# Performance work log

Measured on AMD Instinct MI355X. Metric: run time of the kernel, lower is better.

The kernel has to match this reference:

```python
import jax, jax.numpy as jnp
import numpy as np

B, N, CIN, H, UNITS = 8, 2048, 256, 256, 256


def setup_inputs() -> dict:
    key = jax.random.key(0)
    ks = jax.random.split(key, 7)
    s = 1.0 / np.sqrt(CIN)
    return {
        "x": jax.random.normal(ks[0], (B, N, CIN), dtype=jnp.float32),
        "Wq": jax.random.normal(ks[1], (CIN, H), dtype=jnp.float32) * s,
        "bq": jax.random.normal(ks[2], (H,), dtype=jnp.float32) * 0.01,
        "Wk": jax.random.normal(ks[3], (CIN, H), dtype=jnp.float32) * s,
        "bk": jax.random.normal(ks[4], (H,), dtype=jnp.float32) * 0.01,
        "Wm": jax.random.normal(ks[5], (H, UNITS), dtype=jnp.float32) * (1.0 / np.sqrt(H)),
        "bm": jax.random.normal(ks[6], (UNITS,), dtype=jnp.float32) * 0.01,
    }


def reference(x, Wq, bq, Wk, bk, Wm, bm):
    # Dense projections with fused relu (as in the Keras module)
    q = jax.nn.relu(x @ Wq + bq)          # (B,N,H)
    k = jax.nn.relu(x @ Wk + bk)          # (B,N,H)
    v = q                                 # NOTE: source uses fc_query for value (fc_value unused)
    # Unscaled key @ query^T, softmax over last axis
    kq = jax.nn.softmax(jnp.einsum('bnh,bmh->bnm', k, q), axis=-1)  # (B,N,N)
    # value^T @ kq, then Permute((2,1)): att[b,m,h] = sum_n v[b,n,h] * kq[b,n,m]
    att = jnp.einsum('bnh,bnm->bmh', v, kq)                          # (B,N,H)
    return jax.nn.relu(att @ Wm + bm)                                # (B,N,UNITS)
```

## Files before the change

kernel.cpp:

```cpp
#include <hip/hip_runtime.h>
#include <hip/hip_bf16.h>
#include <math.h>

#define BB   8
#define NN   2048
#define CC   256
#define MTOT (BB * NN)

typedef __bf16 bf16_t;
typedef bf16_t    bf16x8 __attribute__((ext_vector_type(8)));
typedef _Float16  halfx8 __attribute__((ext_vector_type(8)));
typedef float     floatx4 __attribute__((ext_vector_type(4)));

#define LOG2E 1.44269504088896f

__device__ __forceinline__ void gl_lds16(const bf16_t* g, bf16_t* l) {
    __builtin_amdgcn_global_load_lds(
        (const __attribute__((address_space(1))) unsigned int*)g,
        (__attribute__((address_space(3))) unsigned int*)l, 16, 0, 0);
}

template<int OMODE, bool BIASRELU, bool DO_STATS>
__global__ __launch_bounds__(256, 3)
void gemm_nt(const bf16_t* __restrict__ A, const bf16_t* __restrict__ B,
             void* __restrict__ C, const float* __restrict__ bias,
             int lda, int ldb, int ldc,
             long strideA, long strideB, long strideC,
             float* __restrict__ pm, float* __restrict__ pl)
{
    const int b = blockIdx.z;
    A += (long)b * strideA;
    B += (long)b * strideB;
    const int m0 = blockIdx.y * 128;
    const int n0 = blockIdx.x * 128;

    __shared__ bf16_t As[128 * 32];
    __shared__ bf16_t Bs[128 * 32];
    __shared__ float  smx[4][4][16];
    __shared__ float  ssm[4][4][16];

    const int tid  = threadIdx.x;
    const int wid  = tid >> 6, lane = tid & 63;
    const int wm   = (wid >> 1) * 64, wn = (wid & 1) * 64;
    const int fr   = lane & 15;
    const int kb   = (lane >> 4) * 8;

    floatx4 acc[4][4] = {};

    for (int k0 = 0; k0 < 256; k0 += 32) {
#pragma unroll
        for (int r = 0; r < 2; ++r) {
            const int lin = tid + r * 256;
            const int rw  = lin >> 2, kc = lin & 3;
            gl_lds16(A + (long)(m0 + rw) * lda + k0 + kc * 8, As + lin * 8);
            gl_lds16(B + (long)(n0 + rw) * ldb + k0 + kc * 8, Bs + lin * 8);
        }
        __syncthreads();
        bf16x8 af[4], bf[4];
#pragma unroll
        for (int f = 0; f < 4; ++f) {
            af[f] = *(const bf16x8*)(As + (wm + f * 16 + fr) * 32 + kb);
            bf[f] = *(const bf16x8*)(Bs + (wn + f * 16 + fr) * 32 + kb);
        }
#pragma unroll
        for (int f = 0; f < 4; ++f)
#pragma unroll
            for (int g = 0; g < 4; ++g)
                acc[f][g] = __builtin_amdgcn_mfma_f32_16x16x32_bf16(af[f], bf[g], acc[f][g], 0, 0, 0);
        __syncthreads();
    }

    const int rbase = (lane >> 4) * 4;
#pragma unroll
    for (int g = 0; g < 4; ++g) {
        const int n = n0 + wn + g * 16 + fr;
        const float bv = BIASRELU ? bias[n] : 0.0f;
#pragma unroll
        for (int f = 0; f < 4; ++f) {
#pragma unroll
            for (int r = 0; r < 4; ++r) {
                const int m = m0 + wm + f * 16 + rbase + r;
                float v = acc[f][g][r] + bv;
                if (BIASRELU) v = v > 0.0f ? v : 0.0f;
                if (OMODE == 0)
                    ((float*)C)[(long)b * strideC + (long)m * ldc + n] = v;
                else if (OMODE == 1)
                    ((bf16_t*)C)[(long)b * strideC + (long)m * ldc + n] = (bf16_t)v;
                else
                    ((_Float16*)C)[(long)b * strideC + (long)m * ldc + n] = (_Float16)v;
            }
        }
    }

    if (DO_STATS) {
        float lmax[4], lsum[4];
#pragma unroll
        for (int g = 0; g < 4; ++g) {
            float m = -1e30f;
#pragma unroll
            for (int f = 0; f < 4; ++f)
#pragma unroll
                for (int r = 0; r < 4; ++r) m = fmaxf(m, acc[f][g][r]);
            m = fmaxf(m, __shfl_xor(m, 16));
            m = fmaxf(m, __shfl_xor(m, 32));
            float s = 0.0f;
#pragma unroll
            for (int f = 0; f < 4; ++f)
#pragma unroll
                for (int r = 0; r < 4; ++r) s += __expf(acc[f][g][r] - m);
            s += __shfl_xor(s, 16);
            s += __shfl_xor(s, 32);
            lmax[g] = m; lsum[g] = s;
        }
        if (lane < 16) {
#pragma unroll
            for (int g = 0; g < 4; ++g) {
                smx[wid][g][lane] = lmax[g];
                ssm[wid][g][lane] = lsum[g];
            }
        }
        __syncthreads();
        if (tid < 128) {
            const int pair = tid >> 6;
            const int idx  = tid & 63;
            const int g = idx >> 4, f2 = idx & 15;
            const float m0v = smx[pair][g][f2], m1v = smx[pair + 2][g][f2];
            const float M = fmaxf(m0v, m1v);
            const float L = ssm[pair][g][f2] * __expf(m0v - M) +
                            ssm[pair + 2][g][f2] * __expf(m1v - M);
            const int n = n0 + pair * 64 + g * 16 + f2;
            const long o = ((long)b * 16 + blockIdx.y) * NN + n;
            pm[o] = M;
            pl[o] = L;
        }
    }
}

__global__ __launch_bounds__(256)
void stats_combine(const float* __restrict__ pm, const float* __restrict__ pl,
                   float* __restrict__ c2)
{
    const int i = blockIdx.x * 256 + threadIdx.x;
    const int b = i >> 11, n = i & 2047;
    float M = -1e30f, L = 0.0f;
#pragma unroll
    for (int t = 0; t < 16; ++t) {
        const long o = ((long)b * 16 + t) * NN + n;
        const float m = pm[o], l = pl[o];
        const float nm = fmaxf(M, m);
        L = L * __expf(M - nm) + l * __expf(m - nm);
        M = nm;
    }
    c2[i] = (M + logf(L)) * LOG2E;
}

#define APAD 68
__global__ __launch_bounds__(256, 4)
void att_out(const _Float16* __restrict__ St, const bf16_t* __restrict__ qmT,
             const float* __restrict__ c2, const float* __restrict__ bm,
             float* __restrict__ out)
{
    const int b  = blockIdx.z;
    const int m0 = blockIdx.x * 32;
    const int u0 = blockIdx.y * 128;
    const _Float16* S  = St  + (long)b * NN * NN;
    const bf16_t*   Q  = qmT + (long)b * 256 * NN;
    const float*    C2 = c2  + b * NN;
    float*          O  = out + (long)b * NN * 256;

    __shared__ bf16_t As[32 * APAD];
    __shared__ bf16_t Bs[128 * 64];

    const int tid  = threadIdx.x;
    const int wid  = tid >> 6, lane = tid & 63;
    const int wm2  = (wid >> 1) * 16;
    const int wu   = (wid & 1) * 64;
    const int fr   = lane & 15;
    const int u16  = lane >> 4;
    const int kb   = u16 * 8;
    const int fsw  = fr & 7;
    const int arow = tid >> 3;
    const int aseg = tid & 7;

    const _Float16* Srow = S + (long)(m0 + arow) * NN + aseg * 8;

    floatx4 acc[4] = {};

    for (int n0 = 0; n0 < NN; n0 += 64) {
#pragma unroll
        for (int r = 0; r < 4; ++r) {
            const int lin = tid + r * 256;
            const int rw  = lin >> 3, kc = lin & 7;
            const int kcs = kc ^ (rw & 7);
            gl_lds16(Q + (long)(u0 + rw) * NN + n0 + kcs * 8, Bs + lin * 8);
        }
        const halfx8 hv = *(const halfx8*)(Srow + n0);
        const float4 ca = *(const float4*)(C2 + n0 + aseg * 8);
        const float4 cb = *(const float4*)(C2 + n0 + aseg * 8 + 4);
        bf16x8 p;
        p[0] = (bf16_t)exp2f(fmaf((float)hv[0], LOG2E, -ca.x));
        p[1] = (bf16_t)exp2f(fmaf((float)hv[1], LOG2E, -ca.y));
        p[2] = (bf16_t)exp2f(fmaf((float)hv[2], LOG2E, -ca.z));
        p[3] = (bf16_t)exp2f(fmaf((float)hv[3], LOG2E, -ca.w));
        p[4] = (bf16_t)exp2f(fmaf((float)hv[4], LOG2E, -cb.x));
        p[5] = (bf16_t)exp2f(fmaf((float)hv[5], LOG2E, -cb.y));
        p[6] = (bf16_t)exp2f(fmaf((float)hv[6], LOG2E, -cb.z));
        p[7] = (bf16_t)exp2f(fmaf((float)hv[7], LOG2E, -cb.w));
        *(bf16x8*)(As + arow * APAD + aseg * 8) = p;
        __syncthreads();

        bf16x8 af[2], bg[4][2];
#pragma unroll
        for (int j = 0; j < 2; ++j)
            af[j] = *(const bf16x8*)(As + (wm2 + fr) * APAD + j * 32 + kb);
#pragma unroll
        for (int g = 0; g < 4; ++g)
#pragma unroll
            for (int j = 0; j < 2; ++j) {
                const int chunk = (j * 4 + u16) ^ fsw;
                bg[g][j] = *(const bf16x8*)(Bs + (wu + g * 16 + fr) * 64 + chunk * 8);
            }
#pragma unroll
        for (int j = 0; j < 2; ++j)
#pragma unroll
            for (int g = 0; g < 4; ++g)
                acc[g] = __builtin_amdgcn_mfma_f32_16x16x32_bf16(af[j], bg[g][j], acc[g], 0, 0, 0);
        __syncthreads();
    }

    const int rbase = u16 * 4;
#pragma unroll
    for (int g = 0; g < 4; ++g) {
        const int u = u0 + wu + g * 16 + fr;
        const float bvv = bm[u];
#pragma unroll
        for (int r = 0; r < 4; ++r) {
            const int m = m0 + wm2 + rbase + r;
            const float v = acc[g][r] + bvv;
            O[(long)m * 256 + u] = v > 0.0f ? v : 0.0f;
        }
    }
}

__global__ __launch_bounds__(256)
void cvt_bf16(const float* __restrict__ x, bf16_t* __restrict__ y)
{
    const long i = ((long)blockIdx.x * 256 + threadIdx.x) * 8;
    const float4 a = *(const float4*)(x + i);
    const float4 b = *(const float4*)(x + i + 4);
    bf16x8 o;
    o[0] = (bf16_t)a.x; o[1] = (bf16_t)a.y; o[2] = (bf16_t)a.z; o[3] = (bf16_t)a.w;
    o[4] = (bf16_t)b.x; o[5] = (bf16_t)b.y; o[6] = (bf16_t)b.z; o[7] = (bf16_t)b.w;
    *(bf16x8*)(y + i) = o;
}

__global__ __launch_bounds__(256)
void prep_w(const float* __restrict__ Wq, const float* __restrict__ Wk,
            const float* __restrict__ Wm, const float* __restrict__ bq,
            const float* __restrict__ bk, bf16_t* __restrict__ WqkT,
            bf16_t* __restrict__ WmT, float* __restrict__ bqk)
{
    const int z = blockIdx.z;
    const float* W = (z == 0) ? Wq : (z == 1) ? Wk : Wm;
    bf16_t* Wt = (z == 0) ? WqkT : (z == 1) ? (WqkT + 256 * 256) : WmT;
    __shared__ float t[32][33];
    const int n0 = blockIdx.x * 32, k0 = blockIdx.y * 32;
    const int tx = threadIdx.x & 31, ty = threadIdx.x >> 5;
    for (int i = ty; i < 32; i += 8) t[i][tx] = W[(k0 + i) * 256 + n0 + tx];
    __syncthreads();
    for (int i = ty; i < 32; i += 8) Wt[(n0 + i) * 256 + k0 + tx] = (bf16_t)t[tx][i];
    if (z == 0 && blockIdx.x == 0 && blockIdx.y == 0) {
        bqk[threadIdx.x]       = bq[threadIdx.x];
        bqk[256 + threadIdx.x] = bk[threadIdx.x];
    }
}

extern "C" void kernel_launch(void* const* d_in, const int* in_sizes, int n_in,
                              void* d_out, int out_size, void* d_ws, size_t ws_size,
                              hipStream_t stream)
{
    (void)in_sizes; (void)n_in; (void)out_size; (void)ws_size;
    const float* x  = (const float*)d_in[0];
    const float* Wq = (const float*)d_in[1];
    const float* bq = (const float*)d_in[2];
    const float* Wk = (const float*)d_in[3];
    const float* bk = (const float*)d_in[4];
    const float* Wm = (const float*)d_in[5];
    const float* bm = (const float*)d_in[6];
    float* out = (float*)d_out;

    char* w = (char*)d_ws;
    _Float16* St   = (_Float16*)w;                  w += (size_t)BB * NN * NN * 2;
    bf16_t* x_bf   = (bf16_t*)w;                    w += (size_t)MTOT * 256 * 2;
    bf16_t* qk     = (bf16_t*)w;                    w += (size_t)MTOT * 512 * 2;
    bf16_t* qmT    = (bf16_t*)w;                    w += (size_t)MTOT * 256 * 2;
    bf16_t* WqkT   = (bf16_t*)w;                    w += 512 * 256 * 2;
    bf16_t* WmT    = (bf16_t*)w;                    w += 256 * 256 * 2;
    float*  bqk    = (float*)w;                     w += 512 * 4;
    float*  pm     = (float*)w;                     w += (size_t)BB * 16 * NN * 4;
    float*  pl     = (float*)w;                     w += (size_t)BB * 16 * NN * 4;
    float*  c2b    = (float*)w;

    cvt_bf16<<<dim3(MTOT * 256 / (256 * 8)), 256, 0, stream>>>(x, x_bf);
    prep_w<<<dim3(8, 8, 3), 256, 0, stream>>>(Wq, Wk, Wm, bq, bk, WqkT, WmT, bqk);

    gemm_nt<1, true, false><<<dim3(4, 128, 1), 256, 0, stream>>>(
        x_bf, WqkT, qk, bqk, 256, 256, 512, 0, 0, 0, nullptr, nullptr);

    gemm_nt<1, false, false><<<dim3(16, 2, BB), 256, 0, stream>>>(
        WmT, qk, qmT, nullptr, 256, 512, NN,
        0, (long)NN * 512, (long)256 * NN, nullptr, nullptr);

    gemm_nt<2, false, true><<<dim3(16, 16, BB), 256, 0, stream>>>(
        qk, qk + 256, St, nullptr, 512, 512, NN,
        (long)NN * 512, (long)NN * 512, (long)NN * NN, pm, pl);

    stats_combine<<<dim3(MTOT / 256), 256, 0, stream>>>(pm, pl, c2b);

    att_out<<<dim3(64, 2, BB), 256, 0, stream>>>(St, qmT, c2b, bm, out);
}
```

Baseline: 179.6 us.

## Widen GEMM K-tile to 64 with swizzle; cover all 256 units per att_out block

The generic NT GEMM now stages 64-wide K tiles with an XOR-swizzled LDS layout, halving the number of barrier-separated iterations and avoiding bank conflicts. The att_out kernel now computes all 256 output units per block instead of splitting them across two blocks. This means the exp of the score matrix and the St reads are done once rather than twice. The cost is larger LDS and register use, with occupancy hints lowered to 2 blocks per CU, and half as many att_out blocks.

After: 180.1 us. About the same (+0.3%).

```diff
diff --git a/kernel.cpp b/kernel.cpp
--- a/kernel.cpp
+++ b/kernel.cpp
@@ -34,8 +34,8 @@
     const int m0 = blockIdx.y * 128;
     const int n0 = blockIdx.x * 128;
 
-    __shared__ bf16_t As[128 * 32];
-    __shared__ bf16_t Bs[128 * 32];
+    __shared__ bf16_t As[128 * 64];
+    __shared__ bf16_t Bs[128 * 64];
     __shared__ float  smx[4][4][16];
     __shared__ float  ssm[4][4][16];
 
@@ -43,34 +43,41 @@
     const int wid  = tid >> 6, lane = tid & 63;
     const int wm   = (wid >> 1) * 64, wn = (wid & 1) * 64;
     const int fr   = lane & 15;
-    const int kb   = (lane >> 4) * 8;
+    const int u16  = lane >> 4;
+    const int fsw  = fr & 7;
 
     floatx4 acc[4][4] = {};
 
-    for (int k0 = 0; k0 < 256; k0 += 32) {
-#pragma unroll
-        for (int r = 0; r < 2; ++r) {
+    for (int k0 = 0; k0 < 256; k0 += 64) {
+#pragma unroll
+        for (int r = 0; r < 4; ++r) {
             const int lin = tid + r * 256;
-            const int rw  = lin >> 2, kc = lin & 3;
-            gl_lds16(A + (long)(m0 + rw) * lda + k0 + kc * 8, As + lin * 8);
-            gl_lds16(B + (long)(n0 + rw) * ldb + k0 + kc * 8, Bs + lin * 8);
-        }
-        __syncthreads();
-        bf16x8 af[4], bf[4];
-#pragma unroll
-        for (int f = 0; f < 4; ++f) {
-            af[f] = *(const bf16x8*)(As + (wm + f * 16 + fr) * 32 + kb);
-            bf[f] = *(const bf16x8*)(Bs + (wn + f * 16 + fr) * 32 + kb);
-        }
+            const int rw  = lin >> 3, kc = lin & 7;
+            const int kcs = kc ^ (rw & 7);
+            gl_lds16(A + (long)(m0 + rw) * lda + k0 + kcs * 8, As + lin * 8);
+            gl_lds16(B + (long)(n0 + rw) * ldb + k0 + kcs * 8, Bs + lin * 8);
+        }
+        __syncthreads();
+        bf16x8 af[4][2], bf[4][2];
 #pragma unroll
         for (int f = 0; f < 4; ++f)
 #pragma unroll
-            for (int g = 0; g < 4; ++g)
-                acc[f][g] = __builtin_amdgcn_mfma_f32_16x16x32_bf16(af[f], bf[g], acc[f][g], 0, 0, 0);
-        __syncthreads();
-    }
-
-    const int rbase = (lane >> 4) * 4;
+            for (int j = 0; j < 2; ++j) {
+                const int chunk = (j * 4 + u16) ^ fsw;
+                af[f][j] = *(const bf16x8*)(As + (wm + f * 16 + fr) * 64 + chunk * 8);
+                bf[f][j] = *(const bf16x8*)(Bs + (wn + f * 16 + fr) * 64 + chunk * 8);
+            }
+#pragma unroll
+        for (int j = 0; j < 2; ++j)
+#pragma unroll
+            for (int f = 0; f < 4; ++f)
+#pragma unroll
+                for (int g = 0; g < 4; ++g)
+                    acc[f][g] = __builtin_amdgcn_mfma_f32_16x16x32_bf16(af[f][j], bf[g][j], acc[f][g], 0, 0, 0);
+        __syncthreads();
+    }
+
+    const int rbase = u16 * 4;
 #pragma unroll
     for (int g = 0; g < 4; ++g) {
         const int n = n0 + wn + g * 16 + fr;
@@ -155,26 +162,25 @@
 }
 
 #define APAD 68
-__global__ __launch_bounds__(256, 4)
+__global__ __launch_bounds__(256, 2)
 void att_out(const _Float16* __restrict__ St, const bf16_t* __restrict__ qmT,
              const float* __restrict__ c2, const float* __restrict__ bm,
              float* __restrict__ out)
 {
     const int b  = blockIdx.z;
     const int m0 = blockIdx.x * 32;
-    const int u0 = blockIdx.y * 128;
     const _Float16* S  = St  + (long)b * NN * NN;
     const bf16_t*   Q  = qmT + (long)b * 256 * NN;
     const float*    C2 = c2  + b * NN;
     float*          O  = out + (long)b * NN * 256;
 
     __shared__ bf16_t As[32 * APAD];
-    __shared__ bf16_t Bs[128 * 64];
+    __shared__ bf16_t Bs[256 * 64];
 
     const int tid  = threadIdx.x;
     const int wid  = tid >> 6, lane = tid & 63;
     const int wm2  = (wid >> 1) * 16;
-    const int wu   = (wid & 1) * 64;
+    const int wu   = (wid & 1) * 128;
     const int fr   = lane & 15;
     const int u16  = lane >> 4;
     const int kb   = u16 * 8;
@@ -184,15 +190,15 @@
 
     const _Float16* Srow = S + (long)(m0 + arow) * NN + aseg * 8;
 
-    floatx4 acc[4] = {};
+    floatx4 acc[8] = {};
 
     for (int n0 = 0; n0 < NN; n0 += 64) {
 #pragma unroll
-        for (int r = 0; r < 4; ++r) {
+        for (int r = 0; r < 8; ++r) {
             const int lin = tid + r * 256;
             const int rw  = lin >> 3, kc = lin & 7;
             const int kcs = kc ^ (rw & 7);
-            gl_lds16(Q + (long)(u0 + rw) * NN + n0 + kcs * 8, Bs + lin * 8);
+            gl_lds16(Q + (long)rw * NN + n0 + kcs * 8, Bs + lin * 8);
         }
         const halfx8 hv = *(const halfx8*)(Srow + n0);
         const float4 ca = *(const float4*)(C2 + n0 + aseg * 8);
@@ -209,12 +215,12 @@
         *(bf16x8*)(As + arow * APAD + aseg * 8) = p;
         __syncthreads();
 
-        bf16x8 af[2], bg[4][2];
+        bf16x8 af[2], bg[8][2];
 #pragma unroll
         for (int j = 0; j < 2; ++j)
             af[j] = *(const bf16x8*)(As + (wm2 + fr) * APAD + j * 32 + kb);
 #pragma unroll
-        for (int g = 0; g < 4; ++g)
+        for (int g = 0; g < 8; ++g)
 #pragma unroll
             for (int j = 0; j < 2; ++j) {
                 const int chunk = (j * 4 + u16) ^ fsw;
@@ -223,15 +229,15 @@
 #pragma unroll
         for (int j = 0; j < 2; ++j)
 #pragma unroll
-            for (int g = 0; g < 4; ++g)
+            for (int g = 0; g < 8; ++g)
                 acc[g] = __builtin_amdgcn_mfma_f32_16x16x32_bf16(af[j], bg[g][j], acc[g], 0, 0, 0);
         __syncthreads();
     }
 
     const int rbase = u16 * 4;
 #pragma unroll
-    for (int g = 0; g < 4; ++g) {
-        const int u = u0 + wu + g * 16 + fr;
+    for (int g = 0; g < 8; ++g) {
+        const int u = wu + g * 16 + fr;
         const float bvv = bm[u];
 #pragma unroll
         for (int r = 0; r < 4; ++r) {
@@ -317,5 +323,5 @@
 
     stats_combine<<<dim3(MTOT / 256), 256, 0, stream>>>(pm, pl, c2b);
 
-    att_out<<<dim3(64, 2, BB), 256, 0, stream>>>(St, qmT, c2b, bm, out);
-}
+    att_out<<<dim3(64, 1, BB), 256, 0, stream>>>(St, qmT, c2b, bm, out);
+}
```
